# Performance work log

Measured on AMD Instinct MI355X. Metric: run time of the kernel, lower is better.

Reference implementation:

```python
import jax, jax.numpy as jnp
import numpy as np
from jax import lax

N_SAMPLES = 2 ** 15      # 32768
D_SIZE = 256             # number of dictionary atoms
KERNEL = 256             # atom length
N_STEPS = 16             # sparse_coding_iterations
CHANNELS = 128


def setup_inputs() -> dict:
    key = jax.random.key(0)
    ks = jax.random.split(key, 9)
    B = 8
    x = jax.random.normal(ks[0], (B, N_SAMPLES), dtype=jnp.float32)
    # dictionary, initialized uniform(-1, 1) as in nn.Parameter(...).uniform_(-1, 1)
    d = jax.random.uniform(ks[1], (D_SIZE, KERNEL), dtype=jnp.float32, minval=-1.0, maxval=1.0)
    # 1x1 Conv1d weights stored as (out, in); biases (out,)
    w_pos_amp = jax.random.normal(ks[2], (CHANNELS, 2), dtype=jnp.float32) * 0.1
    b_pos_amp = jnp.zeros((CHANNELS,), dtype=jnp.float32)
    w_atoms = jax.random.normal(ks[3], (CHANNELS, D_SIZE), dtype=jnp.float32) * 0.05
    b_atoms = jnp.zeros((CHANNELS,), dtype=jnp.float32)
    w_reduce = jax.random.normal(ks[4], (CHANNELS, 2 * CHANNELS), dtype=jnp.float32) * 0.05
    b_reduce = jnp.zeros((CHANNELS,), dtype=jnp.float32)
    return {
        'x': x, 'd': d,
        'w_pos_amp': w_pos_amp, 'b_pos_amp': b_pos_amp,
        'w_atoms': w_atoms, 'b_atoms': b_atoms,
        'w_reduce': w_reduce, 'b_reduce': b_reduce,
    }


def _correlate(residual, d):
    # residual: (B, 1, N), d: (D, K) -> feature map (B, D, N-K+1) (valid cross-correlation,
    # identical to torch F.conv1d with no padding)
    return lax.conv_general_dilated(
        residual, d[:, None, :], window_strides=(1,), padding='VALID',
        dimension_numbers=('NCH', 'OIH', 'NCH'))


def _matching_pursuit(x3, d):
    """16-step greedy matching pursuit. Returns key points (B, 2+D, N_STEPS) and residual."""
    B = x3.shape[0]
    T = N_SAMPLES - KERNEL + 1  # valid correlation length

    def step(residual, _):
        fm = _correlate(residual, d)                       # (B, D, T)
        flat = fm.reshape(B, -1)
        idx = jnp.argmax(jnp.abs(flat), axis=1)            # best (atom, pos) per example
        amp = jnp.take_along_axis(flat, idx[:, None], axis=1)[:, 0]
        atom_idx = idx // T
        pos = idx % T

        def subtract(r, p, ai, a):
            seg = lax.dynamic_slice(r, (p,), (KERNEL,))
            return lax.dynamic_update_slice(r, seg - a * d[ai], (p,))

        new_res = jax.vmap(subtract)(residual[:, 0, :], pos, atom_idx, amp)[:, None, :]
        enc = jnp.concatenate([
            (pos.astype(jnp.float32) / T)[:, None],        # normalized position
            amp[:, None],                                  # amplitude
            jax.nn.one_hot(atom_idx, D_SIZE, dtype=jnp.float32),  # atom one-hot
        ], axis=1)                                         # (B, 2+D)
        return new_res, enc

    residual, encs = lax.scan(step, x3, None, length=N_STEPS)  # encs: (S, B, 2+D)
    kp = jnp.transpose(encs, (1, 2, 0))                        # (B, 2+D, S)
    return kp, residual


def _conv1x1(w, b, x):
    # w: (O, C), x: (B, C, T) -> (B, O, T)
    return jnp.einsum('oc,bct->bot', w, x) + b[None, :, None]


def reference(x, d, w_pos_amp, b_pos_amp, w_atoms, b_atoms, w_reduce, b_reduce):
    B = x.shape[0]
    x3 = x.reshape(B, 1, N_SAMPLES)
    kp, _ = _matching_pursuit(x3, d)          # (B, 258, 16)
    pos_amp = kp[:, :2, :]
    atoms = kp[:, 2:, :]
    pa = _conv1x1(w_pos_amp, b_pos_amp, pos_amp)
    at = _conv1x1(w_atoms, b_atoms, atoms)
    h = jnp.concatenate([pa, at], axis=1)     # (B, 2*channels, 16)
    return _conv1x1(w_reduce, b_reduce, h)    # (B, channels, 16)
```

## Files before the change

kernel.cpp:

```cpp
#include <hip/hip_runtime.h>
#include <hip/hip_bf16.h>
#include <float.h>

#define NS 32768
#define KER 256
#define TOUT 32513
#define NATOM 256
#define NSTEP 16
#define BATCH 8
#define NBLK 255
#define XSTR 33024
#define SW4(i) ((i) + (((i) >> 5) << 2))

typedef __attribute__((ext_vector_type(8))) _Float16 half8;
typedef __attribute__((ext_vector_type(16))) float f32x16;
typedef __attribute__((ext_vector_type(4))) unsigned int uint4v;

__device__ __forceinline__ void cmax(float& ba, float& bs, float& bi,
                                     float oa, float os, float oi) {
    if (oa > ba || (oa == ba && oi < bi)) { ba = oa; bs = os; bi = oi; }
}

__device__ __forceinline__ void fma8(float acc[8], float4 dA, float4 dB,
                                     float4 w0, float4 w1, float4 w2, float4 w3) {
    float w[16] = {w0.x,w0.y,w0.z,w0.w, w1.x,w1.y,w1.z,w1.w,
                   w2.x,w2.y,w2.z,w2.w, w3.x,w3.y,w3.z,w3.w};
    float dv[8] = {dA.x,dA.y,dA.z,dA.w, dB.x,dB.y,dB.z,dB.w};
#pragma unroll
    for (int i = 0; i < 8; ++i)
#pragma unroll
        for (int j = 0; j < 8; ++j)
            acc[j] = fmaf(dv[i], w[i + j], acc[j]);
}

__device__ __forceinline__ unsigned short f16hi(float v) {
    return __builtin_bit_cast(unsigned short, (_Float16)v);
}
__device__ __forceinline__ unsigned short f16lo(float v) {
    const _Float16 h = (_Float16)v;
    return __builtin_bit_cast(unsigned short, (_Float16)(v - (float)h));
}

__global__ __launch_bounds__(256) void k_prep(const float* __restrict__ x,
                                              const float* __restrict__ d,
                                              uint2* __restrict__ xh4,
                                              uint2* __restrict__ xl4,
                                              uint4* __restrict__ dhF,
                                              uint4* __restrict__ dlF) {
    const int gid = blockIdx.x * 256 + threadIdx.x;
    const int NXE = BATCH * XSTR;
    if (gid < NXE) {
        const int b = gid / XSTR, i = gid - b * XSTR;
        float v[4];
#pragma unroll
        for (int u = 0; u < 4; ++u)
            v[u] = (i + u < NS) ? x[b * NS + i + u] : 0.f;
        uint2 hw, lw;
        hw.x = (unsigned int)f16hi(v[0]) | ((unsigned int)f16hi(v[1]) << 16);
        hw.y = (unsigned int)f16hi(v[2]) | ((unsigned int)f16hi(v[3]) << 16);
        lw.x = (unsigned int)f16lo(v[0]) | ((unsigned int)f16lo(v[1]) << 16);
        lw.y = (unsigned int)f16lo(v[2]) | ((unsigned int)f16lo(v[3]) << 16);
        xh4[gid] = hw; xl4[gid] = lw;
    } else {
        const int j = gid - NXE;
        if (j < NATOM * 32) {
            const int kg = j >> 8, atom = j & 255;
            const float* dp = d + atom * 256 + (kg << 3);
            uint4 hw, lw;
            hw.x = (unsigned int)f16hi(dp[0]) | ((unsigned int)f16hi(dp[1]) << 16);
            hw.y = (unsigned int)f16hi(dp[2]) | ((unsigned int)f16hi(dp[3]) << 16);
            hw.z = (unsigned int)f16hi(dp[4]) | ((unsigned int)f16hi(dp[5]) << 16);
            hw.w = (unsigned int)f16hi(dp[6]) | ((unsigned int)f16hi(dp[7]) << 16);
            lw.x = (unsigned int)f16lo(dp[0]) | ((unsigned int)f16lo(dp[1]) << 16);
            lw.y = (unsigned int)f16lo(dp[2]) | ((unsigned int)f16lo(dp[3]) << 16);
            lw.z = (unsigned int)f16lo(dp[4]) | ((unsigned int)f16lo(dp[5]) << 16);
            lw.w = (unsigned int)f16lo(dp[6]) | ((unsigned int)f16lo(dp[7]) << 16);
            dhF[(kg << 8) + atom] = hw;
            dlF[(kg << 8) + atom] = lw;
        }
    }
}

__global__ __launch_bounds__(256) void k_init(const uint2* __restrict__ xh4,
                                              const uint2* __restrict__ xl4,
                                              const uint4* __restrict__ dhF,
                                              const uint4* __restrict__ dlF,
                                              float2* __restrict__ bm) {
    const int c = blockIdx.x, mg = blockIdx.y, b = blockIdx.z;
    const int tid = threadIdx.x;
    const int w = tid >> 6, l = tid & 63;
    const int n = l & 31, h = l >> 5;
    __shared__ uint2 xh[512], xl[512];
    __shared__ float4 wmax[4][32];
    const int t0 = c << 8;
    for (int i = tid; i < 512; i += 256) {
        xh[i] = xh4[b * XSTR + t0 + i];
        xl[i] = xl4[b * XSTR + t0 + i];
    }
    __syncthreads();

    const int arow = (mg << 5) + n;
    f32x16 acc0 = {0.f}, acc1 = {0.f};
#pragma unroll
    for (int j = 0; j < 16; ++j) { acc0[j] = 0.f; acc1[j] = 0.f; }
    const int sb = (w << 6) + n + (h << 3);
#pragma unroll 2
    for (int kk = 0; kk < 16; ++kk) {
        const int kg = (kk << 1) + h;
        const half8 ah = __builtin_bit_cast(half8, dhF[(kg << 8) + arow]);
        const half8 al = __builtin_bit_cast(half8, dlF[(kg << 8) + arow]);
        const int s0 = sb + (kk << 4);
        {
            const uint2 h0 = xh[s0], h1 = xh[s0 + 4];
            const uint2 l0 = xl[s0], l1 = xl[s0 + 4];
            const uint4v hv = {h0.x, h0.y, h1.x, h1.y};
            const uint4v lv = {l0.x, l0.y, l1.x, l1.y};
            const half8 bh = __builtin_bit_cast(half8, hv);
            const half8 bl = __builtin_bit_cast(half8, lv);
            acc0 = __builtin_amdgcn_mfma_f32_32x32x16_f16(ah, bl, acc0, 0, 0, 0);
            acc0 = __builtin_amdgcn_mfma_f32_32x32x16_f16(al, bh, acc0, 0, 0, 0);
            acc0 = __builtin_amdgcn_mfma_f32_32x32x16_f16(ah, bh, acc0, 0, 0, 0);
        }
        {
            const uint2 h0 = xh[s0 + 32], h1 = xh[s0 + 36];
            const uint2 l0 = xl[s0 + 32], l1 = xl[s0 + 36];
            const uint4v hv = {h0.x, h0.y, h1.x, h1.y};
            const uint4v lv = {l0.x, l0.y, l1.x, l1.y};
            const half8 bh = __builtin_bit_cast(half8, hv);
            const half8 bl = __builtin_bit_cast(half8, lv);
            acc1 = __builtin_amdgcn_mfma_f32_32x32x16_f16(ah, bl, acc1, 0, 0, 0);
            acc1 = __builtin_amdgcn_mfma_f32_32x32x16_f16(al, bh, acc1, 0, 0, 0);
            acc1 = __builtin_amdgcn_mfma_f32_32x32x16_f16(ah, bh, acc1, 0, 0, 0);
        }
    }

    const int tb0 = t0 + (w << 6) + n;
#pragma unroll
    for (int r = 0; r < 16; ++r) {
        const int atom_l = (r & 3) + ((r >> 2) << 3) + (h << 2);
        const float fa = (float)(((mg << 5) + atom_l) * TOUT);
        float ba = -1.f, bsg = 0.f, bi = 3.0e7f;
        const float v0 = acc0[r], v1 = acc1[r];
        if (tb0 < TOUT) { ba = fabsf(v0); bsg = v0; bi = fa + (float)tb0; }
        if (tb0 + 32 < TOUT) {
            const float a1 = fabsf(v1);
            if (a1 > ba) { ba = a1; bsg = v1; bi = fa + (float)(tb0 + 32); }
        }
#pragma unroll
        for (int m = 1; m <= 16; m <<= 1) {
            const float oa = __shfl_xor(ba, m, 32);
            const float os = __shfl_xor(bsg, m, 32);
            const float oi = __shfl_xor(bi, m, 32);
            cmax(ba, bsg, bi, oa, os, oi);
        }
        if (n == 0) wmax[w][atom_l] = make_float4(ba, bsg, bi, 0.f);
    }
    __syncthreads();
    if (tid < 64) {
        const int a = tid & 31, p = tid >> 5;
        const float4 e1 = wmax[(p << 1)][a];
        const float4 e2 = wmax[(p << 1) + 1][a];
        float ba = e1.x, bsg = e1.y, bi = e1.z;
        cmax(ba, bsg, bi, e2.x, e2.y, e2.z);
        const int blk = (c << 1) + p;
        if (blk < NBLK)
            bm[(size_t)((b << 8) + (mg << 5) + a) * NBLK + blk] = make_float2(bsg, bi);
    }
}

__global__ __launch_bounds__(256) void k_lvl2(const float2* __restrict__ bm,
                                              float4* __restrict__ l2) {
    const int b = blockIdx.y;
    const int oglob = blockIdx.x * 8 + (threadIdx.x >> 5);
    const int lane = threadIdx.x & 31;
    const float2* row = bm + (size_t)(b * NATOM + oglob) * NBLK;
    float ba = -1.f, bsg = 0.f, bi = 3.0e7f;
    for (int i = lane; i < NBLK; i += 32) {
        const float2 e = row[i];
        cmax(ba, bsg, bi, fabsf(e.x), e.x, e.y);
    }
#pragma unroll
    for (int m = 16; m >= 1; m >>= 1) {
        const float oa = __shfl_xor(ba, m, 32);
        const float os = __shfl_xor(bsg, m, 32);
        const float oi = __shfl_xor(bi, m, 32);
        cmax(ba, bsg, bi, oa, os, oi);
    }
    if (lane == 0) l2[(b << 8) + oglob] = make_float4(ba, bsg, bi, 0.f);
}

__global__ __launch_bounds__(512) void k_step(const float* __restrict__ d,
                                              const float* __restrict__ resid_src,
                                              float* __restrict__ resid_dst,
                                              float2* __restrict__ bm,
                                              float4* __restrict__ l2,
                                              int* __restrict__ pos_a,
                                              int* __restrict__ atom_a,
                                              float* __restrict__ amp_a,
                                              int step) {
    const int og = blockIdx.x, b = blockIdx.y;
    const int tid = threadIdx.x;
    const int wave = tid >> 6, lane = tid & 63;
    __shared__ float dt[2048];
    __shared__ float rsu[1024];
    __shared__ float4 sred[8];
    __shared__ float4 upd[8][5];
    __shared__ int sh_pos, sh_atom;
    __shared__ float sh_amp;

    ((float4*)dt)[tid] = ((const float4*)(d + og * 2048))[tid];
    const float4* l2r = l2 + (step & 1) * (BATCH * NATOM);
    float4*       l2w = l2 + ((step + 1) & 1) * (BATCH * NATOM);

    {
        float ba = -1.f, bsg = 0.f, bi = 3.0e7f;
        if (tid < 256) {
            const float4 e = l2r[(b << 8) + tid];
            ba = e.x; bsg = e.y; bi = e.z;
        }
#pragma unroll
        for (int m = 32; m >= 1; m >>= 1) {
            const float oa = __shfl_xor(ba, m);
            const float os = __shfl_xor(bsg, m);
            const float oi = __shfl_xor(bi, m);
            cmax(ba, bsg, bi, oa, os, oi);
        }
        if (lane == 0) sred[wave] = make_float4(ba, bsg, bi, 0.f);
    }
    __syncthreads();
    if (tid == 0) {
        float4 r = sred[0];
#pragma unroll
        for (int i = 1; i < 8; ++i) {
            const float4 q = sred[i];
            if (q.x > r.x || (q.x == r.x && q.z < r.z)) r = q;
        }
        const int idx = (int)r.z;
        const int atom = idx / TOUT;
        const int pos = idx - atom * TOUT;
        sh_pos = pos; sh_atom = atom; sh_amp = r.y;
        if (og == 0) {
            pos_a[step * BATCH + b] = pos;
            atom_a[step * BATCH + b] = atom;
            amp_a[step * BATCH + b] = r.y;
        }
    }
    __syncthreads();
    const int p = sh_pos, atom_s = sh_atom;
    const float amp = sh_amp;

    for (int i = tid; i < 1024; i += 512) {
        const int g = (og << 10) + i;
        float v = resid_src[(size_t)b * NS + g];
        const int off = g - p;
        if (off >= 0 && off < KER)
            v = __fsub_rn(v, __fmul_rn(amp, d[atom_s * KER + off]));
        resid_dst[(size_t)b * NS + g] = v;
    }

    int tlo = p - 255; if (tlo < 0) tlo = 0;
    int thi = p + 255; if (thi > TOUT - 1) thi = TOUT - 1;
    const int bs0 = tlo >> 7, be0 = thi >> 7;
    const int rbase = bs0 << 7;
    const int nblks = be0 - bs0 + 1;
    const int rlen = (nblks << 7) + 255;
    for (int i = tid; i < rlen; i += 512) {
        const int g = rbase + i;
        float v = (g < NS) ? resid_src[(size_t)b * NS + g] : 0.f;
        const int off = g - p;
        if (g < NS && off >= 0 && off < KER)
            v = __fsub_rn(v, __fmul_rn(amp, d[atom_s * KER + off]));
        rsu[SW4(i)] = v;
    }
    __syncthreads();

    const int lg = lane >> 4, l16 = lane & 15;
    const float* dp = dt + (wave << 8) + (lg << 6);
    const int atomg = (og << 3) + wave;
    for (int bb = 0; bb < nblks; ++bb) {
        const int blk = bs0 + bb;
        const int t0r = (bb << 7) + (l16 << 3) + (lg << 6);
        float acc[8];
#pragma unroll
        for (int j = 0; j < 8; ++j) acc[j] = 0.f;
        float4 A0 = *(const float4*)(rsu + SW4(t0r));
        float4 A1 = *(const float4*)(rsu + SW4(t0r + 4));
        float4 B0 = *(const float4*)(rsu + SW4(t0r + 8));
        float4 B1 = *(const float4*)(rsu + SW4(t0r + 12));
#pragma unroll
        for (int kk = 0; kk < 64; kk += 16) {
            const float4 d0 = *(const float4*)(dp + kk);
            const float4 d1 = *(const float4*)(dp + kk + 4);
            const float4 N0 = *(const float4*)(rsu + SW4(t0r + kk + 16));
            const float4 N1 = *(const float4*)(rsu + SW4(t0r + kk + 20));
            fma8(acc, d0, d1, A0, A1, B0, B1);
            const float4 d2 = *(const float4*)(dp + kk + 8);
            const float4 d3 = *(const float4*)(dp + kk + 12);
            const float4 M0 = *(const float4*)(rsu + SW4(t0r + kk + 24));
            const float4 M1 = *(const float4*)(rsu + SW4(t0r + kk + 28));
            fma8(acc, d2, d3, B0, B1, N0, N1);
            A0 = N0; A1 = N1; B0 = M0; B1 = M1;
        }
#pragma unroll
        for (int j = 0; j < 8; ++j) {
            acc[j] += __shfl_xor(acc[j], 16);
            acc[j] += __shfl_xor(acc[j], 32);
        }
        float ba = -1.f, bsg = 0.f, bi = 3.0e7f;
        const int tbp = rbase + (bb << 7) + (l16 << 3);
#pragma unroll
        for (int j = 0; j < 8; ++j) {
            const int t = tbp + j;
            const float av = fabsf(acc[j]);
            if (t < TOUT && av > ba) { ba = av; bsg = acc[j]; bi = (float)(atomg * TOUT + t); }
        }
#pragma unroll
        for (int m = 32; m >= 1; m >>= 1) {
            const float oa = __shfl_xor(ba, m);
            const float os = __shfl_xor(bsg, m);
            const float oi = __shfl_xor(bi, m);
            cmax(ba, bsg, bi, oa, os, oi);
        }
        if (lane == 0) {
            bm[(size_t)(b * NATOM + atomg) * NBLK + blk] = make_float2(bsg, bi);
            upd[wave][bb] = make_float4(ba, bsg, bi, 0.f);
        }
    }
    __syncthreads();

    {
        float ba = -1.f, bsg = 0.f, bi = 3.0e7f;
        const float2* row = bm + (size_t)(b * NATOM + atomg) * NBLK;
        for (int i = lane; i < NBLK; i += 64) {
            if (i >= bs0 && i <= be0) {
                const float4 e2 = upd[wave][i - bs0];
                cmax(ba, bsg, bi, e2.x, e2.y, e2.z);
            } else {
                const float2 e2 = row[i];
                cmax(ba, bsg, bi, fabsf(e2.x), e2.x, e2.y);
            }
        }
#pragma unroll
        for (int m = 32; m >= 1; m >>= 1) {
            const float oa = __shfl_xor(ba, m);
            const float os = __shfl_xor(bsg, m);
            const float oi = __shfl_xor(bi, m);
            cmax(ba, bsg, bi, oa, os, oi);
        }
        if (lane == 0) l2w[(b << 8) + atomg] = make_float4(ba, bsg, bi, 0.f);
    }
}

__global__ __launch_bounds__(128) void k_head(const int* __restrict__ pos_a,
                                              const int* __restrict__ atom_a,
                                              const float* __restrict__ amp_a,
                                              const float4* __restrict__ l2,
                                              const float* __restrict__ wpa,
                                              const float* __restrict__ bpa,
                                              const float* __restrict__ wat,
                                              const float* __restrict__ bat,
                                              const float* __restrict__ wr,
                                              const float* __restrict__ br,
                                              float* __restrict__ out) {
    const int s = blockIdx.x, b = blockIdx.y;
    const int o = threadIdx.x;
    __shared__ float4 hred[2];
    __shared__ int sh_pos, sh_atom;
    __shared__ float sh_amp;
    int pos, atom; float amp;
    if (s == NSTEP - 1) {
        const float4* l2r = l2 + ((NSTEP - 1) & 1) * (BATCH * NATOM);
        float ba = -1.f, bsg = 0.f, bi = 3.0e7f;
        const float4 e0 = l2r[(b << 8) + o];
        const float4 e1 = l2r[(b << 8) + 128 + o];
        cmax(ba, bsg, bi, e0.x, e0.y, e0.z);
        cmax(ba, bsg, bi, e1.x, e1.y, e1.z);
#pragma unroll
        for (int m = 32; m >= 1; m >>= 1) {
            const float oa = __shfl_xor(ba, m);
            const float os = __shfl_xor(bsg, m);
            const float oi = __shfl_xor(bi, m);
            cmax(ba, bsg, bi, oa, os, oi);
        }
        if ((o & 63) == 0) hred[o >> 6] = make_float4(ba, bsg, bi, 0.f);
        __syncthreads();
        if (o == 0) {
            float4 r = hred[0];
            const float4 q = hred[1];
            if (q.x > r.x || (q.x == r.x && q.z < r.z)) r = q;
            const int idx = (int)r.z;
            sh_atom = idx / TOUT;
            sh_pos = idx - sh_atom * TOUT;
            sh_amp = r.y;
        }
        __syncthreads();
        pos = sh_pos; atom = sh_atom; amp = sh_amp;
    } else {
        pos  = pos_a[s * BATCH + b];
        atom = atom_a[s * BATCH + b];
        amp  = amp_a[s * BATCH + b];
    }
    const float posn = (float)pos / 32513.0f;
    float sum = br[o];
    for (int c = 0; c < 128; ++c) {
        const float pa = wpa[c * 2] * posn + wpa[c * 2 + 1] * amp + bpa[c];
        const float at = wat[c * 256 + atom] + bat[c];
        sum += wr[o * 256 + c] * pa + wr[o * 256 + 128 + c] * at;
    }
    out[(b * 128 + o) * NSTEP + s] = sum;
}

extern "C" void kernel_launch(void* const* d_in, const int* in_sizes, int n_in,
                              void* d_out, int out_size, void* d_ws, size_t ws_size,
                              hipStream_t stream) {
    const float* x   = (const float*)d_in[0];
    const float* d   = (const float*)d_in[1];
    const float* wpa = (const float*)d_in[2];
    const float* bpa = (const float*)d_in[3];
    const float* wat = (const float*)d_in[4];
    const float* bat = (const float*)d_in[5];
    const float* wr  = (const float*)d_in[6];
    const float* br  = (const float*)d_in[7];
    float* out = (float*)d_out;

    char* ws = (char*)d_ws;
    float2* bm     = (float2*)ws;
    float4* l2     = (float4*)(ws + 4177920);
    int*    pos_a  = (int*)(ws + 4243456);
    int*    atom_a = (int*)(ws + 4243968);
    float*  amp_a  = (float*)(ws + 4244480);
    float*  resid0 = (float*)(ws + 4244992);
    float*  resid1 = (float*)(ws + 5293568);
    uint2*  xh4    = (uint2*)(ws + 6342144);
    uint2*  xl4    = (uint2*)(ws + 8455680);
    uint4*  dhF    = (uint4*)(ws + 10569216);
    uint4*  dlF    = (uint4*)(ws + 10700288);

    hipMemcpyAsync(resid0, x, (size_t)BATCH * NS * sizeof(float),
                   hipMemcpyDeviceToDevice, stream);
    const int prep_n = BATCH * XSTR + NATOM * 32;
    k_prep<<<(prep_n + 255) / 256, 256, 0, stream>>>(x, d, xh4, xl4, dhF, dlF);
    k_init<<<dim3(128, 8, 8), 256, 0, stream>>>(xh4, xl4, dhF, dlF, bm);
    k_lvl2<<<dim3(32, 8), 256, 0, stream>>>(bm, l2);
    for (int st = 0; st < NSTEP - 1; ++st) {
        float* rs = (st & 1) ? resid1 : resid0;
        float* rd = (st & 1) ? resid0 : resid1;
        k_step<<<dim3(32, 8), 512, 0, stream>>>(d, rs, rd, bm, l2,
                                                pos_a, atom_a, amp_a, st);
    }
    k_head<<<dim3(16, 8), 128, 0, stream>>>(pos_a, atom_a, amp_a, l2,
                                            wpa, bpa, wat, bat, wr, br, out);
}
```

Baseline: 443.2 us.

## Enlarge k_init MFMA tile and interleave hi/lo f16 signal into one buffer

The initial full correlation kernel now has each wave compute a 64-atom by 128-position tile instead of 32x64. This reuses each loaded dictionary fragment across four position tiles and halves the grid. The hi and lo f16 halves of the signal are packed into a single uint4 array, so the shared-memory loads are 16-byte reads. The per-block max is written straight from each wave, dropping the shared-memory second reduction and one barrier. The workspace is rearranged so the packed signal buffer aliases resid0, and the residual copy is moved after the init kernels. The larger tile raises register pressure and may lower occupancy.

```diff
diff --git a/kernel.cpp b/kernel.cpp
--- a/kernel.cpp
+++ b/kernel.cpp
@@ -43,8 +43,7 @@
 
 __global__ __launch_bounds__(256) void k_prep(const float* __restrict__ x,
                                               const float* __restrict__ d,
-                                              uint2* __restrict__ xh4,
-                                              uint2* __restrict__ xl4,
+                                              uint4* __restrict__ xhl4,
                                               uint4* __restrict__ dhF,
                                               uint4* __restrict__ dlF) {
     const int gid = blockIdx.x * 256 + threadIdx.x;
@@ -55,12 +54,12 @@
 #pragma unroll
         for (int u = 0; u < 4; ++u)
             v[u] = (i + u < NS) ? x[b * NS + i + u] : 0.f;
-        uint2 hw, lw;
-        hw.x = (unsigned int)f16hi(v[0]) | ((unsigned int)f16hi(v[1]) << 16);
-        hw.y = (unsigned int)f16hi(v[2]) | ((unsigned int)f16hi(v[3]) << 16);
-        lw.x = (unsigned int)f16lo(v[0]) | ((unsigned int)f16lo(v[1]) << 16);
-        lw.y = (unsigned int)f16lo(v[2]) | ((unsigned int)f16lo(v[3]) << 16);
-        xh4[gid] = hw; xl4[gid] = lw;
+        uint4 q;
+        q.x = (unsigned int)f16hi(v[0]) | ((unsigned int)f16hi(v[1]) << 16);
+        q.y = (unsigned int)f16hi(v[2]) | ((unsigned int)f16hi(v[3]) << 16);
+        q.z = (unsigned int)f16lo(v[0]) | ((unsigned int)f16lo(v[1]) << 16);
+        q.w = (unsigned int)f16lo(v[2]) | ((unsigned int)f16lo(v[3]) << 16);
+        xhl4[gid] = q;
     } else {
         const int j = gid - NXE;
         if (j < NATOM * 32) {
@@ -81,8 +80,7 @@
     }
 }
 
-__global__ __launch_bounds__(256) void k_init(const uint2* __restrict__ xh4,
-                                              const uint2* __restrict__ xl4,
+__global__ __launch_bounds__(256) void k_init(const uint4* __restrict__ xhl4,
                                               const uint4* __restrict__ dhF,
                                               const uint4* __restrict__ dlF,
                                               float2* __restrict__ bm) {
@@ -90,81 +88,73 @@
     const int tid = threadIdx.x;
     const int w = tid >> 6, l = tid & 63;
     const int n = l & 31, h = l >> 5;
-    __shared__ uint2 xh[512], xl[512];
-    __shared__ float4 wmax[4][32];
-    const int t0 = c << 8;
-    for (int i = tid; i < 512; i += 256) {
-        xh[i] = xh4[b * XSTR + t0 + i];
-        xl[i] = xl4[b * XSTR + t0 + i];
-    }
+    __shared__ uint4 xw[768];
+    const int t0 = c << 9;
+    for (int i = tid; i < 768; i += 256)
+        xw[i] = xhl4[b * XSTR + t0 + i];
     __syncthreads();
 
-    const int arow = (mg << 5) + n;
-    f32x16 acc0 = {0.f}, acc1 = {0.f};
-#pragma unroll
-    for (int j = 0; j < 16; ++j) { acc0[j] = 0.f; acc1[j] = 0.f; }
-    const int sb = (w << 6) + n + (h << 3);
+    f32x16 acc[2][4];
+#pragma unroll
+    for (int mt = 0; mt < 2; ++mt)
+#pragma unroll
+        for (int nt = 0; nt < 4; ++nt)
+#pragma unroll
+            for (int j = 0; j < 16; ++j) acc[mt][nt][j] = 0.f;
+
+    const int abase = (mg << 6) + n;
+    const int sbb = (w << 7) + n + (h << 3);
 #pragma unroll 2
     for (int kk = 0; kk < 16; ++kk) {
         const int kg = (kk << 1) + h;
-        const half8 ah = __builtin_bit_cast(half8, dhF[(kg << 8) + arow]);
-        const half8 al = __builtin_bit_cast(half8, dlF[(kg << 8) + arow]);
-        const int s0 = sb + (kk << 4);
-        {
-            const uint2 h0 = xh[s0], h1 = xh[s0 + 4];
-            const uint2 l0 = xl[s0], l1 = xl[s0 + 4];
-            const uint4v hv = {h0.x, h0.y, h1.x, h1.y};
-            const uint4v lv = {l0.x, l0.y, l1.x, l1.y};
+        const half8 ah0 = __builtin_bit_cast(half8, dhF[(kg << 8) + abase]);
+        const half8 al0 = __builtin_bit_cast(half8, dlF[(kg << 8) + abase]);
+        const half8 ah1 = __builtin_bit_cast(half8, dhF[(kg << 8) + abase + 32]);
+        const half8 al1 = __builtin_bit_cast(half8, dlF[(kg << 8) + abase + 32]);
+#pragma unroll
+        for (int nt = 0; nt < 4; ++nt) {
+            const int s0 = sbb + (nt << 5) + (kk << 4);
+            const uint4 q0 = xw[s0], q1 = xw[s0 + 4];
+            const uint4v hv = {q0.x, q0.y, q1.x, q1.y};
+            const uint4v lv = {q0.z, q0.w, q1.z, q1.w};
             const half8 bh = __builtin_bit_cast(half8, hv);
             const half8 bl = __builtin_bit_cast(half8, lv);
-            acc0 = __builtin_amdgcn_mfma_f32_32x32x16_f16(ah, bl, acc0, 0, 0, 0);
-            acc0 = __builtin_amdgcn_mfma_f32_32x32x16_f16(al, bh, acc0, 0, 0, 0);
-            acc0 = __builtin_amdgcn_mfma_f32_32x32x16_f16(ah, bh, acc0, 0, 0, 0);
-        }
-        {
-            const uint2 h0 = xh[s0 + 32], h1 = xh[s0 + 36];
-            const uint2 l0 = xl[s0 + 32], l1 = xl[s0 + 36];
-            const uint4v hv = {h0.x, h0.y, h1.x, h1.y};
-            const uint4v lv = {l0.x, l0.y, l1.x, l1.y};
-            const half8 bh = __builtin_bit_cast(half8, hv);
-            const half8 bl = __builtin_bit_cast(half8, lv);
-            acc1 = __builtin_amdgcn_mfma_f32_32x32x16_f16(ah, bl, acc1, 0, 0, 0);
-            acc1 = __builtin_amdgcn_mfma_f32_32x32x16_f16(al, bh, acc1, 0, 0, 0);
-            acc1 = __builtin_amdgcn_mfma_f32_32x32x16_f16(ah, bh, acc1, 0, 0, 0);
-        }
-    }
-
-    const int tb0 = t0 + (w << 6) + n;
-#pragma unroll
-    for (int r = 0; r < 16; ++r) {
-        const int atom_l = (r & 3) + ((r >> 2) << 3) + (h << 2);
-        const float fa = (float)(((mg << 5) + atom_l) * TOUT);
-        float ba = -1.f, bsg = 0.f, bi = 3.0e7f;
-        const float v0 = acc0[r], v1 = acc1[r];
-        if (tb0 < TOUT) { ba = fabsf(v0); bsg = v0; bi = fa + (float)tb0; }
-        if (tb0 + 32 < TOUT) {
-            const float a1 = fabsf(v1);
-            if (a1 > ba) { ba = a1; bsg = v1; bi = fa + (float)(tb0 + 32); }
-        }
-#pragma unroll
-        for (int m = 1; m <= 16; m <<= 1) {
-            const float oa = __shfl_xor(ba, m, 32);
-            const float os = __shfl_xor(bsg, m, 32);
-            const float oi = __shfl_xor(bi, m, 32);
-            cmax(ba, bsg, bi, oa, os, oi);
-        }
-        if (n == 0) wmax[w][atom_l] = make_float4(ba, bsg, bi, 0.f);
-    }
-    __syncthreads();
-    if (tid < 64) {
-        const int a = tid & 31, p = tid >> 5;
-        const float4 e1 = wmax[(p << 1)][a];
-        const float4 e2 = wmax[(p << 1) + 1][a];
-        float ba = e1.x, bsg = e1.y, bi = e1.z;
-        cmax(ba, bsg, bi, e2.x, e2.y, e2.z);
-        const int blk = (c << 1) + p;
-        if (blk < NBLK)
-            bm[(size_t)((b << 8) + (mg << 5) + a) * NBLK + blk] = make_float2(bsg, bi);
+            acc[0][nt] = __builtin_amdgcn_mfma_f32_32x32x16_f16(ah0, bl, acc[0][nt], 0, 0, 0);
+            acc[0][nt] = __builtin_amdgcn_mfma_f32_32x32x16_f16(al0, bh, acc[0][nt], 0, 0, 0);
+            acc[0][nt] = __builtin_amdgcn_mfma_f32_32x32x16_f16(ah0, bh, acc[0][nt], 0, 0, 0);
+            acc[1][nt] = __builtin_amdgcn_mfma_f32_32x32x16_f16(ah1, bl, acc[1][nt], 0, 0, 0);
+            acc[1][nt] = __builtin_amdgcn_mfma_f32_32x32x16_f16(al1, bh, acc[1][nt], 0, 0, 0);
+            acc[1][nt] = __builtin_amdgcn_mfma_f32_32x32x16_f16(ah1, bh, acc[1][nt], 0, 0, 0);
+        }
+    }
+
+    const int blk = (c << 2) + w;
+    if (blk < NBLK) {
+#pragma unroll
+        for (int mt = 0; mt < 2; ++mt) {
+#pragma unroll
+            for (int r = 0; r < 16; ++r) {
+                const int atom = (mg << 6) + (mt << 5) + (r & 3) + (((r >> 2)) << 3) + (h << 2);
+                const float fa = (float)(atom * TOUT);
+                float ba = -1.f, bsg = 0.f, bi = 3.0e7f;
+#pragma unroll
+                for (int nt = 0; nt < 4; ++nt) {
+                    const int t = t0 + (w << 7) + (nt << 5) + n;
+                    const float v = acc[mt][nt][r];
+                    const float av = fabsf(v);
+                    if (t < TOUT && av > ba) { ba = av; bsg = v; bi = fa + (float)t; }
+                }
+#pragma unroll
+                for (int m = 1; m <= 16; m <<= 1) {
+                    const float oa = __shfl_xor(ba, m, 32);
+                    const float os = __shfl_xor(bsg, m, 32);
+                    const float oi = __shfl_xor(bi, m, 32);
+                    cmax(ba, bsg, bi, oa, os, oi);
+                }
+                if (n == 0)
+                    bm[(size_t)((b << 8) + atom) * NBLK + blk] = make_float2(bsg, bi);
+            }
+        }
     }
 }
 
@@ -429,19 +419,18 @@
     int*    pos_a  = (int*)(ws + 4243456);
     int*    atom_a = (int*)(ws + 4243968);
     float*  amp_a  = (float*)(ws + 4244480);
-    float*  resid0 = (float*)(ws + 4244992);
-    float*  resid1 = (float*)(ws + 5293568);
-    uint2*  xh4    = (uint2*)(ws + 6342144);
-    uint2*  xl4    = (uint2*)(ws + 8455680);
-    uint4*  dhF    = (uint4*)(ws + 10569216);
-    uint4*  dlF    = (uint4*)(ws + 10700288);
-
+    uint4*  dhF    = (uint4*)(ws + 4244992);
+    uint4*  dlF    = (uint4*)(ws + 4376064);
+    uint4*  xhl4   = (uint4*)(ws + 4507136);
+    float*  resid0 = (float*)(ws + 4507136);
+    float*  resid1 = (float*)(ws + 5555712);
+
+    const int prep_n = BATCH * XSTR + NATOM * 32;
+    k_prep<<<(prep_n + 255) / 256, 256, 0, stream>>>(x, d, xhl4, dhF, dlF);
+    k_init<<<dim3(64, 4, 8), 256, 0, stream>>>(xhl4, dhF, dlF, bm);
+    k_lvl2<<<dim3(32, 8), 256, 0, stream>>>(bm, l2);
     hipMemcpyAsync(resid0, x, (size_t)BATCH * NS * sizeof(float),
                    hipMemcpyDeviceToDevice, stream);
-    const int prep_n = BATCH * XSTR + NATOM * 32;
-    k_prep<<<(prep_n + 255) / 256, 256, 0, stream>>>(x, d, xh4, xl4, dhF, dlF);
-    k_init<<<dim3(128, 8, 8), 256, 0, stream>>>(xh4, xl4, dhF, dlF, bm);
-    k_lvl2<<<dim3(32, 8), 256, 0, stream>>>(bm, l2);
     for (int st = 0; st < NSTEP - 1; ++st) {
         float* rs = (st & 1) ? resid1 : resid0;
         float* rd = (st & 1) ? resid0 : resid1;
```

Measured after the change: 509.9 us. 15.0% more time.
